# Kernel optimization log

Hardware: AMD Instinct MI355X
Metric: run time of the kernel (lower is better)

The kernel has to match this reference:

```python
import jax, jax.numpy as jnp
import numpy as np

O, T, H, W = 512, 1024, 16, 16
DIN, DP, HID, DOUT = 64, 64, 128, 128


def conv2d(x, w, b):
    # 'same' padding, stride 1, NCHW / OIHW
    ph, pw = w.shape[2] // 2, w.shape[3] // 2
    y = jax.lax.conv_general_dilated(
        x, w, (1, 1), [(ph, ph), (pw, pw)],
        dimension_numbers=('NCHW', 'OIHW', 'NCHW'))
    return y + b[None, :, None, None]


def inorm(x):
    # nn.InstanceNorm2d (affine=False), biased variance, eps=1e-5
    m = jnp.mean(x, axis=(2, 3), keepdims=True)
    v = jnp.mean((x - m) ** 2, axis=(2, 3), keepdims=True)
    return (x - m) * jax.lax.rsqrt(v + 1e-5)


def lrelu(x):
    return jnp.where(x >= 0, x, 0.1 * x)


def block(x, w, b):
    # conv -> InstanceNorm -> LeakyReLU(0.1)
    return lrelu(inorm(conv2d(x, w, b)))


def setup_inputs() -> dict:
    key = jax.random.key(0)
    ks = jax.random.split(key, 12)

    def rn(k, shape):
        fan_in = shape[1] * shape[2] * shape[3]
        return jax.random.normal(k, shape, dtype=jnp.float32) / np.sqrt(fan_in)

    return {
        'obj_maps': jax.random.normal(ks[0], (O, DIN, H, W), jnp.float32),
        'pred_vecs': jax.random.normal(ks[1], (T, DP), jnp.float32),
        'edges': jax.random.randint(ks[2], (T, 2), 0, O),
        'obj_to_img': jax.random.randint(ks[3], (O,), 0, 8),
        # net1_2d: C3 (2*DIN+DP -> HID) + IN + LReLU ; C3 (HID -> 2*HID+DOUT) no act
        'w1a': rn(ks[4], (HID, 2 * DIN + DP, 3, 3)), 'b1a': jnp.zeros((HID,), jnp.float32),
        'w1b': rn(ks[5], (2 * HID + DOUT, HID, 3, 3)), 'b1b': jnp.zeros((2 * HID + DOUT,), jnp.float32),
        # net2_2d: C3 (HID -> HID) act ; C1 (HID -> DOUT) act (non_linear_activated)
        'w2a': rn(ks[6], (HID, HID, 3, 3)), 'b2a': jnp.zeros((HID,), jnp.float32),
        'w2b': rn(ks[7], (DOUT, HID, 1, 1)), 'b2b': jnp.zeros((DOUT,), jnp.float32),
        # net_obj: C3 (DIN -> HID) act ; C1 (HID -> DOUT) act
        'woa': rn(ks[8], (HID, DIN, 3, 3)), 'boa': jnp.zeros((HID,), jnp.float32),
        'wob': rn(ks[9], (DOUT, HID, 1, 1)), 'bob': jnp.zeros((DOUT,), jnp.float32),
    }


def reference(obj_maps, pred_vecs, edges, obj_to_img,
              w1a, b1a, w1b, b1b, w2a, b2a, w2b, b2b, woa, boa, wob, bob):
    s_idx = edges[:, 0]
    o_idx = edges[:, 1]
    # pred vecs broadcast to (T, DP, H, W)
    p = jnp.broadcast_to(pred_vecs[:, :, None, None], (T, DP, H, W))
    # gather object maps by edge endpoints, concat channelwise
    t = jnp.concatenate([obj_maps[s_idx], p, obj_maps[o_idx]], axis=1)
    t = block(t, w1a, b1a)
    t = conv2d(t, w1b, b1b)  # last conv of net1_2d has no norm/activation
    new_s = t[:, :HID]                                # subject messages
    new_p = lrelu(inorm(t[:, HID:HID + DOUT]))        # self.activation branch
    new_o = t[:, HID + DOUT:]                         # object messages
    # scatter-add pooling back to objects, then average
    pooled = (jax.ops.segment_sum(new_s, s_idx, num_segments=O)
              + jax.ops.segment_sum(new_o, o_idx, num_segments=O))
    ones = jnp.ones((T,), obj_maps.dtype)
    counts = (jax.ops.segment_sum(ones, s_idx, num_segments=O)
              + jax.ops.segment_sum(ones, o_idx, num_segments=O))
    pooled = pooled / jnp.maximum(counts, 1.0)[:, None, None, None]
    new_obj = (block(block(pooled, w2a, b2a), w2b, b2b)
               + block(block(obj_maps, woa, boa), wob, bob))
    return new_obj, new_p
```

## Files before the change

kernel.cpp:

```cpp
#include <hip/hip_runtime.h>
#include <hip/hip_bf16.h>

typedef __hip_bfloat16 bf16;
typedef __attribute__((ext_vector_type(8))) short short8;
typedef __attribute__((ext_vector_type(4))) float float4v;

#define TPB 256

__device__ __forceinline__ short f2bs(float v) {
    __hip_bfloat16 h = __float2bfloat16(v);
    return *reinterpret_cast<short*>(&h);
}
__device__ __forceinline__ float bs2f(short s) {
    union { unsigned u; float f; } c; c.u = ((unsigned)(unsigned short)s) << 16; return c.f;
}
__device__ __forceinline__ short ldbits(const bf16* p, size_t i)  { return ((const short*)p)[i]; }
__device__ __forceinline__ short ldbits(const float* p, size_t i) { return f2bs(p[i]); }

__device__ __forceinline__ void gl_lds16(const void* g, void* l) {
    __builtin_amdgcn_global_load_lds(
        (const __attribute__((address_space(1))) void*)g,
        (__attribute__((address_space(3))) void*)l, 16, 0, 0);
}

__global__ void wxform_kernel(const float* __restrict__ w, bf16* __restrict__ dst,
                              int Cin, int taps, int total8) {
    int i = blockIdx.x * TPB + threadIdx.x;
    if (i >= total8) return;
    int base = i * 8;
    int nc  = Cin >> 5;
    int ci0 = base % 40;
    int r   = base / 40;
    int nn  = r & 63; r >>= 6;
    int tap = r % taps; r /= taps;
    int cb  = r % nc;
    int nb  = r / nc;
    short8 o;
#pragma unroll
    for (int j = 0; j < 8; ++j) {
        int ci = ci0 + j;
        float v = (ci < 32)
            ? w[((size_t)(nb * 64 + nn) * Cin + (cb * 32 + ci)) * taps + tap] : 0.f;
        o[j] = f2bs(v);
    }
    *(short8*)(dst + base) = o;
}

__global__ void cvt_kernel(const float* __restrict__ src, bf16* __restrict__ dst, int n8) {
    int i = blockIdx.x * TPB + threadIdx.x;
    if (i >= n8) return;
    const float4v* s = (const float4v*)src;
    float4v a = s[i * 2], b = s[i * 2 + 1];
    short8 o;
#pragma unroll
    for (int j = 0; j < 4; ++j) { o[j] = f2bs(a[j]); o[4 + j] = f2bs(b[j]); }
    *(short8*)(dst + (size_t)i * 8) = o;
}

template<int K, int MODE, bool GATHER, int NCB, typename TIN, typename TOUT>
__global__ __launch_bounds__(TPB, 2) void mconv_kernel(
    const TIN* __restrict__ in,
    const float* __restrict__ pred_vecs,
    const int*  __restrict__ edges,
    const bf16* __restrict__ wbf,
    const float* __restrict__ bfp,
    TOUT* __restrict__ out,
    bf16* __restrict__ out_s,
    bf16* __restrict__ out_o,
    int Cin, int Cout)
{
    constexpr int P    = K / 2;
    constexpr int W    = 16 + 2 * P;
    constexpr int TAPS = K * K;
    constexpr int CS   = 40;

    __shared__ __align__(16) short Ash[W * W * CS];
    __shared__ __align__(16) short Bsh[TAPS * 64 * CS];
    __shared__ float redS[256], redS2[256];

    const int tid  = threadIdx.x;
    const int lane = tid & 63;
    const int wv   = tid >> 6;
    const int quad = lane >> 4;
    const int l16  = lane & 15;

    const int d = blockIdx.x;
    const int u = (d & 7) * (gridDim.x >> 3) + (d >> 3);
    const int n  = u / NCB;
    const int n0 = (u - n * NCB) * 64;

    for (int i = tid; i < W * W * CS / 2; i += TPB) ((int*)Ash)[i] = 0;

    float4v acc[4][4];
#pragma unroll
    for (int nt = 0; nt < 4; ++nt) {
        float b = bfp[n0 + nt * 16 + l16];
#pragma unroll
        for (int mt = 0; mt < 4; ++mt) acc[mt][nt] = float4v{b, b, b, b};
    }

    int s_idx = 0, o_idx = 0;
    if (GATHER) { s_idx = edges[2 * n]; o_idx = edges[2 * n + 1]; }

    const int y0 = tid >> 4, x0 = tid & 15;
    const int abase = ((y0 + P) * W + (x0 + P)) * CS;
    const int nc = Cin >> 5;

    for (int cc0 = 0; cc0 < Cin; cc0 += 32) {
        __syncthreads();

        const char* wsrc = (const char*)wbf +
            ((size_t)(n0 >> 6) * nc + (cc0 >> 5)) * (size_t)(TAPS * 64 * CS * 2);
        for (int k = wv; k < TAPS * 5; k += 4)
            gl_lds16(wsrc + (k << 10) + (lane << 4), (char*)Bsh + (k << 10));

#pragma unroll
        for (int c8 = 0; c8 < 4; ++c8) {
            short8 pk;
#pragma unroll
            for (int j = 0; j < 8; ++j) {
                const int gc = cc0 + c8 * 8 + j;
                short s;
                if (GATHER) {
                    if (gc < 64)
                        s = ldbits(in, (size_t)s_idx * 16384 + (size_t)gc * 256 + tid);
                    else if (gc < 128)
                        s = f2bs(pred_vecs[n * 64 + (gc - 64)]);
                    else
                        s = ldbits(in, (size_t)o_idx * 16384 + (size_t)(gc - 128) * 256 + tid);
                } else {
                    s = ldbits(in, ((size_t)n * Cin + gc) * 256 + tid);
                }
                pk[j] = s;
            }
            *(short8*)&Ash[abase + c8 * 8] = pk;
        }
        __syncthreads();

#pragma unroll 1
        for (int tap = 0; tap < TAPS; ++tap) {
            const int dy = (K == 3) ? tap / 3 : 0;
            const int dx = (K == 3) ? tap - dy * 3 : 0;
            short8 bfr[4];
#pragma unroll
            for (int nt = 0; nt < 4; ++nt)
                bfr[nt] = *(const short8*)&Bsh[(tap * 64 + nt * 16 + l16) * CS + quad * 8];
#pragma unroll
            for (int mt = 0; mt < 4; ++mt) {
                const int m = (wv << 6) + mt * 16 + l16;
                const int pix = ((m >> 4) + dy) * W + ((m & 15) + dx);
                short8 afr = *(const short8*)&Ash[pix * CS + quad * 8];
#pragma unroll
                for (int nt = 0; nt < 4; ++nt)
                    acc[mt][nt] = __builtin_amdgcn_mfma_f32_16x16x32_bf16(
                        afr, bfr[nt], acc[mt][nt], 0, 0, 0);
            }
        }
    }

    const bool do_norm = (MODE == 2) ? (n0 >= 128 && n0 < 256) : true;
    float mean[4], rstd[4];
    if (do_norm) {
#pragma unroll
        for (int nt = 0; nt < 4; ++nt) {
            float s = 0.f, s2 = 0.f;
#pragma unroll
            for (int mt = 0; mt < 4; ++mt)
#pragma unroll
                for (int r = 0; r < 4; ++r) {
                    float v = acc[mt][nt][r];
                    s += v; s2 += v * v;
                }
            s  += __shfl_xor(s, 16, 64);  s  += __shfl_xor(s, 32, 64);
            s2 += __shfl_xor(s2, 16, 64); s2 += __shfl_xor(s2, 32, 64);
            if (quad == 0) {
                redS [wv * 64 + nt * 16 + l16] = s;
                redS2[wv * 64 + nt * 16 + l16] = s2;
            }
        }
        __syncthreads();
#pragma unroll
        for (int nt = 0; nt < 4; ++nt) {
            int c = nt * 16 + l16;
            float s  = redS [c] + redS [64 + c] + redS [128 + c] + redS [192 + c];
            float s2 = redS2[c] + redS2[64 + c] + redS2[128 + c] + redS2[192 + c];
            float m  = s * (1.f / 256.f);
            float var = s2 * (1.f / 256.f) - m * m;
            mean[nt] = m;
            rstd[nt] = rsqrtf(var + 1e-5f);
        }
    }

    float* Tb = (float*)Ash;
    constexpr int TS = 264;

    auto store_b = [&](bf16* base, int ch_off) {
#pragma unroll
        for (int s = 0; s < 2; ++s) {
            int task = tid + (s << 8);
            int ch = task >> 5;
            int ck = task & 31;
            const float* src = &Tb[ch * TS + (ck << 3)];
            short8 o;
#pragma unroll
            for (int j = 0; j < 8; ++j) o[j] = f2bs(src[j]);
            *(short8*)(base + (size_t)(ch_off + ch) * 256 + (ck << 3)) = o;
        }
    };
    auto store_f = [&](float* base, int ch_off, bool rmw) {
#pragma unroll
        for (int s = 0; s < 4; ++s) {
            int task = tid + (s << 8);
            int ch = task >> 6;
            int ck = task & 63;
            float4v v = *(const float4v*)&Tb[ch * TS + (ck << 2)];
            float4v* dst = (float4v*)(base + (size_t)(ch_off + ch) * 256) + ck;
            if (rmw) v = v + *dst;
            *dst = v;
        }
    };

#pragma unroll 1
    for (int nt = 0; nt < 4; ++nt) {
        __syncthreads();
#pragma unroll
        for (int mt = 0; mt < 4; ++mt)
#pragma unroll
            for (int r = 0; r < 4; ++r) {
                float v = acc[mt][nt][r];
                if (do_norm) {
                    v = (v - mean[nt]) * rstd[nt];
                    v = (v >= 0.f) ? v : 0.1f * v;
                }
                Tb[l16 * TS + (wv << 6) + mt * 16 + (quad << 2) + r] = v;
            }
        __syncthreads();
        const int nt16 = nt * 16;
        if (MODE == 2) {
            if (n0 < 128)
                store_b(out_s + (size_t)n * 128 * 256, n0 + nt16);
            else if (n0 < 256)
                store_f((float*)out + (size_t)n * 128 * 256, (n0 - 128) + nt16, false);
            else
                store_b(out_o + (size_t)n * 128 * 256, (n0 - 256) + nt16);
        } else if (MODE == 1) {
            store_f((float*)out + (size_t)n * Cout * 256, n0 + nt16, true);
        } else {
            if constexpr (sizeof(TOUT) == 2)
                store_b((bf16*)out + (size_t)n * Cout * 256, n0 + nt16);
            else
                store_f((float*)out + (size_t)n * Cout * 256, n0 + nt16, false);
        }
    }
}

__global__ __launch_bounds__(TPB) void pool_kernel(
    const int* __restrict__ edges,
    const bf16* __restrict__ new_s,
    const bf16* __restrict__ new_o,
    bf16* __restrict__ pooled)
{
    const int ob  = blockIdx.x;
    const int tid = threadIdx.x;
    __shared__ int list[2048];
    __shared__ int cnt;
    if (tid == 0) cnt = 0;
    __syncthreads();
    for (int t = tid; t < 1024; t += TPB) {
        int si = edges[2 * t], oi = edges[2 * t + 1];
        if (si == ob) { int p = atomicAdd(&cnt, 1); list[p] = t * 2; }
        if (oi == ob) { int p = atomicAdd(&cnt, 1); list[p] = t * 2 + 1; }
    }
    __syncthreads();
    const int c = cnt;
    const float inv = 1.f / fmaxf((float)c, 1.f);
    for (int e8 = tid; e8 < 4096; e8 += TPB) {
        float s[8] = {0.f, 0.f, 0.f, 0.f, 0.f, 0.f, 0.f, 0.f};
        for (int m = 0; m < c; ++m) {
            int ent = list[m];
            int nn  = ent >> 1;
            const bf16* src = (ent & 1) ? new_o : new_s;
            short8 v = *(const short8*)(src + (size_t)nn * 32768 + (size_t)e8 * 8);
#pragma unroll
            for (int j = 0; j < 8; ++j) s[j] += bs2f(v[j]);
        }
        short8 o;
#pragma unroll
        for (int j = 0; j < 8; ++j) o[j] = f2bs(s[j] * inv);
        *(short8*)(pooled + (size_t)ob * 32768 + (size_t)e8 * 8) = o;
    }
}

extern "C" void kernel_launch(void* const* d_in, const int* in_sizes, int n_in,
                              void* d_out, int out_size, void* d_ws, size_t ws_size,
                              hipStream_t stream) {
    const float* obj_maps  = (const float*)d_in[0];
    const float* pred_vecs = (const float*)d_in[1];
    const int*   edges     = (const int*)d_in[2];
    const float* w1a = (const float*)d_in[4];  const float* b1a = (const float*)d_in[5];
    const float* w1b = (const float*)d_in[6];  const float* b1b = (const float*)d_in[7];
    const float* w2a = (const float*)d_in[8];  const float* b2a = (const float*)d_in[9];
    const float* w2b = (const float*)d_in[10]; const float* b2b = (const float*)d_in[11];
    const float* woa = (const float*)d_in[12]; const float* boa = (const float*)d_in[13];
    const float* wob = (const float*)d_in[14]; const float* bob = (const float*)d_in[15];

    float* out = (float*)d_out;
    const size_t NP_OFF = (size_t)512 * 128 * 256;

    char* ws = (char*)d_ws;
    size_t off = 0;
    auto alloc = [&](size_t bytes) -> char* {
        char* p = ws + off;
        off += (bytes + 255) & ~(size_t)255;
        return p;
    };
    const size_t SZ_T = (size_t)1024 * 128 * 256 * 2;
    char* Bt1   = alloc(SZ_T);
    char* Bnews = alloc(SZ_T);
    char* Bnewo = alloc(SZ_T);
    auto wsz = [](int Cout, int Cin, int taps) -> size_t {
        return (size_t)(Cout / 64) * (Cin / 32) * taps * 64 * 40 * 2;
    };
    bf16* wb1a = (bf16*)alloc(wsz(128, 192, 9));
    bf16* wb1b = (bf16*)alloc(wsz(384, 128, 9));
    bf16* wb2a = (bf16*)alloc(wsz(128, 128, 9));
    bf16* wb2b = (bf16*)alloc(wsz(128, 128, 1));
    bf16* wboa = (bf16*)alloc(wsz(128,  64, 9));
    bf16* wbob = (bf16*)alloc(wsz(128, 128, 1));
    const size_t OBJ_SZ = (size_t)512 * 64 * 256 * 2;
    bf16* obj_bf = (bf16*)alloc(OBJ_SZ);
    const bool use_objbf = (off <= ws_size);

    bf16* t1     = (bf16*)Bt1;
    bf16* new_s  = (bf16*)Bnews;
    bf16* new_o  = (bf16*)Bnewo;
    bf16* pooled = (bf16*)Bt1;
    bf16* u1     = (bf16*)(Bt1 + (size_t)512 * 128 * 256 * 2);
    bf16* v1     = (bf16*)Bnews;

    auto wx = [&](const float* w, bf16* dw, int Cout, int Cin, int taps) {
        int total8 = (Cout / 64) * (Cin / 32) * taps * 64 * 40 / 8;
        wxform_kernel<<<dim3((total8 + TPB - 1) / TPB), dim3(TPB), 0, stream>>>(
            w, dw, Cin, taps, total8);
    };
    wx(w1a, wb1a, 128, 192, 9);
    wx(w1b, wb1b, 384, 128, 9);
    wx(w2a, wb2a, 128, 128, 9);
    wx(w2b, wb2b, 128, 128, 1);
    wx(woa, wboa, 128,  64, 9);
    wx(wob, wbob, 128, 128, 1);
    if (use_objbf)
        cvt_kernel<<<dim3(4096), dim3(TPB), 0, stream>>>(obj_maps, obj_bf, 512 * 64 * 256 / 8);

    if (use_objbf)
        mconv_kernel<3, 0, true, 2, bf16, bf16><<<dim3(2048), dim3(TPB), 0, stream>>>(
            obj_bf, pred_vecs, edges, wb1a, b1a, t1, nullptr, nullptr, 192, 128);
    else
        mconv_kernel<3, 0, true, 2, float, bf16><<<dim3(2048), dim3(TPB), 0, stream>>>(
            obj_maps, pred_vecs, edges, wb1a, b1a, t1, nullptr, nullptr, 192, 128);

    mconv_kernel<3, 2, false, 6, bf16, float><<<dim3(6144), dim3(TPB), 0, stream>>>(
        t1, nullptr, nullptr, wb1b, b1b, out + NP_OFF, new_s, new_o, 128, 384);

    pool_kernel<<<dim3(512), dim3(TPB), 0, stream>>>(edges, new_s, new_o, pooled);

    mconv_kernel<3, 0, false, 2, bf16, bf16><<<dim3(1024), dim3(TPB), 0, stream>>>(
        pooled, nullptr, nullptr, wb2a, b2a, u1, nullptr, nullptr, 128, 128);

    mconv_kernel<1, 0, false, 2, bf16, float><<<dim3(1024), dim3(TPB), 0, stream>>>(
        u1, nullptr, nullptr, wb2b, b2b, out, nullptr, nullptr, 128, 128);

    if (use_objbf)
        mconv_kernel<3, 0, false, 2, bf16, bf16><<<dim3(1024), dim3(TPB), 0, stream>>>(
            obj_bf, nullptr, nullptr, wboa, boa, v1, nullptr, nullptr, 64, 128);
    else
        mconv_kernel<3, 0, false, 2, float, bf16><<<dim3(1024), dim3(TPB), 0, stream>>>(
            obj_maps, nullptr, nullptr, wboa, boa, v1, nullptr, nullptr, 64, 128);

    mconv_kernel<1, 1, false, 2, bf16, float><<<dim3(1024), dim3(TPB), 0, stream>>>(
        v1, nullptr, nullptr, wbob, bob, out, nullptr, nullptr, 128, 128);
}
```

Measured before the change: 1.416 ms.

## Fuse scatter-add pooling into conv epilogue via float atomics

Measured after the change: 1.779 ms. 1.26x slower.

```diff
diff --git a/kernel.cpp b/kernel.cpp
--- a/kernel.cpp
+++ b/kernel.cpp
@@ -3,6 +3,7 @@
 
 typedef __hip_bfloat16 bf16;
 typedef __attribute__((ext_vector_type(8))) short short8;
+typedef __attribute__((ext_vector_type(4))) short short4v;
 typedef __attribute__((ext_vector_type(4))) float float4v;
 
 #define TPB 256
@@ -10,9 +11,6 @@
 __device__ __forceinline__ short f2bs(float v) {
     __hip_bfloat16 h = __float2bfloat16(v);
     return *reinterpret_cast<short*>(&h);
-}
-__device__ __forceinline__ float bs2f(short s) {
-    union { unsigned u; float f; } c; c.u = ((unsigned)(unsigned short)s) << 16; return c.f;
 }
 __device__ __forceinline__ short ldbits(const bf16* p, size_t i)  { return ((const short*)p)[i]; }
 __device__ __forceinline__ short ldbits(const float* p, size_t i) { return f2bs(p[i]); }
@@ -57,7 +55,21 @@
     *(short8*)(dst + (size_t)i * 8) = o;
 }
 
-template<int K, int MODE, bool GATHER, int NCB, typename TIN, typename TOUT>
+__global__ void counts_kernel(const int* __restrict__ edges, float* __restrict__ invc) {
+    __shared__ int cnt[512];
+    const int tid = threadIdx.x;
+    cnt[tid] = 0; cnt[tid + 256] = 0;
+    __syncthreads();
+    for (int t = tid; t < 1024; t += TPB) {
+        atomicAdd(&cnt[edges[2 * t]], 1);
+        atomicAdd(&cnt[edges[2 * t + 1]], 1);
+    }
+    __syncthreads();
+    invc[tid]       = 1.f / fmaxf((float)cnt[tid], 1.f);
+    invc[tid + 256] = 1.f / fmaxf((float)cnt[tid + 256], 1.f);
+}
+
+template<int K, int MODE, bool GATHER, bool SCALE, int NCB, typename TIN, typename TOUT>
 __global__ __launch_bounds__(TPB, 2) void mconv_kernel(
     const TIN* __restrict__ in,
     const float* __restrict__ pred_vecs,
@@ -65,8 +77,8 @@
     const bf16* __restrict__ wbf,
     const float* __restrict__ bfp,
     TOUT* __restrict__ out,
-    bf16* __restrict__ out_s,
-    bf16* __restrict__ out_o,
+    float* __restrict__ psum,
+    const float* __restrict__ iscale,
     int Cin, int Cout)
 {
     constexpr int P    = K / 2;
@@ -100,7 +112,9 @@
     }
 
     int s_idx = 0, o_idx = 0;
-    if (GATHER) { s_idx = edges[2 * n]; o_idx = edges[2 * n + 1]; }
+    if (GATHER || MODE == 2) { s_idx = edges[2 * n]; o_idx = edges[2 * n + 1]; }
+    float sc = 1.f;
+    if constexpr (SCALE) sc = iscale[n];
 
     const int y0 = tid >> 4, x0 = tid & 15;
     const int abase = ((y0 + P) * W + (x0 + P)) * CS;
@@ -128,6 +142,8 @@
                         s = f2bs(pred_vecs[n * 64 + (gc - 64)]);
                     else
                         s = ldbits(in, (size_t)o_idx * 16384 + (size_t)(gc - 128) * 256 + tid);
+                } else if (SCALE) {
+                    s = f2bs(((const float*)in)[((size_t)n * Cin + gc) * 256 + tid] * sc);
                 } else {
                     s = ldbits(in, ((size_t)n * Cin + gc) * 256 + tid);
                 }
@@ -192,31 +208,37 @@
     }
 
     float* Tb = (float*)Ash;
-    constexpr int TS = 264;
+    constexpr int TS = 260;
 
     auto store_b = [&](bf16* base, int ch_off) {
 #pragma unroll
-        for (int s = 0; s < 2; ++s) {
-            int task = tid + (s << 8);
-            int ch = task >> 5;
-            int ck = task & 31;
-            const float* src = &Tb[ch * TS + (ck << 3)];
-            short8 o;
-#pragma unroll
-            for (int j = 0; j < 8; ++j) o[j] = f2bs(src[j]);
-            *(short8*)(base + (size_t)(ch_off + ch) * 256 + (ck << 3)) = o;
+        for (int s = 0; s < 4; ++s) {
+            const int ch = (s << 2) + wv;
+            const float* src = &Tb[ch * TS + (lane << 2)];
+            short4v o4;
+#pragma unroll
+            for (int j = 0; j < 4; ++j) o4[j] = f2bs(src[j]);
+            *(short4v*)(base + (size_t)(ch_off + ch) * 256 + (lane << 2)) = o4;
         }
     };
     auto store_f = [&](float* base, int ch_off, bool rmw) {
 #pragma unroll
         for (int s = 0; s < 4; ++s) {
-            int task = tid + (s << 8);
-            int ch = task >> 6;
-            int ck = task & 63;
-            float4v v = *(const float4v*)&Tb[ch * TS + (ck << 2)];
-            float4v* dst = (float4v*)(base + (size_t)(ch_off + ch) * 256) + ck;
+            const int ch = (s << 2) + wv;
+            float4v v = *(const float4v*)&Tb[ch * TS + (lane << 2)];
+            float4v* dst = (float4v*)(base + (size_t)(ch_off + ch) * 256) + lane;
             if (rmw) v = v + *dst;
             *dst = v;
+        }
+    };
+    auto atomic_f = [&](float* base, int ch_off) {
+#pragma unroll
+        for (int s = 0; s < 4; ++s) {
+            const int ch = (s << 2) + wv;
+            const float* src = &Tb[ch * TS + (lane << 2)];
+            float* dst = base + (size_t)(ch_off + ch) * 256 + (lane << 2);
+#pragma unroll
+            for (int j = 0; j < 4; ++j) atomicAdd(dst + j, src[j]);
         }
     };
 
@@ -238,11 +260,11 @@
         const int nt16 = nt * 16;
         if (MODE == 2) {
             if (n0 < 128)
-                store_b(out_s + (size_t)n * 128 * 256, n0 + nt16);
+                atomic_f(psum + (size_t)s_idx * 128 * 256, n0 + nt16);
             else if (n0 < 256)
                 store_f((float*)out + (size_t)n * 128 * 256, (n0 - 128) + nt16, false);
             else
-                store_b(out_o + (size_t)n * 128 * 256, (n0 - 256) + nt16);
+                atomic_f(psum + (size_t)o_idx * 128 * 256, (n0 - 256) + nt16);
         } else if (MODE == 1) {
             store_f((float*)out + (size_t)n * Cout * 256, n0 + nt16, true);
         } else {
@@ -251,43 +273,6 @@
             else
                 store_f((float*)out + (size_t)n * Cout * 256, n0 + nt16, false);
         }
-    }
-}
-
-__global__ __launch_bounds__(TPB) void pool_kernel(
-    const int* __restrict__ edges,
-    const bf16* __restrict__ new_s,
-    const bf16* __restrict__ new_o,
-    bf16* __restrict__ pooled)
-{
-    const int ob  = blockIdx.x;
-    const int tid = threadIdx.x;
-    __shared__ int list[2048];
-    __shared__ int cnt;
-    if (tid == 0) cnt = 0;
-    __syncthreads();
-    for (int t = tid; t < 1024; t += TPB) {
-        int si = edges[2 * t], oi = edges[2 * t + 1];
-        if (si == ob) { int p = atomicAdd(&cnt, 1); list[p] = t * 2; }
-        if (oi == ob) { int p = atomicAdd(&cnt, 1); list[p] = t * 2 + 1; }
-    }
-    __syncthreads();
-    const int c = cnt;
-    const float inv = 1.f / fmaxf((float)c, 1.f);
-    for (int e8 = tid; e8 < 4096; e8 += TPB) {
-        float s[8] = {0.f, 0.f, 0.f, 0.f, 0.f, 0.f, 0.f, 0.f};
-        for (int m = 0; m < c; ++m) {
-            int ent = list[m];
-            int nn  = ent >> 1;
-            const bf16* src = (ent & 1) ? new_o : new_s;
-            short8 v = *(const short8*)(src + (size_t)nn * 32768 + (size_t)e8 * 8);
-#pragma unroll
-            for (int j = 0; j < 8; ++j) s[j] += bs2f(v[j]);
-        }
-        short8 o;
-#pragma unroll
-        for (int j = 0; j < 8; ++j) o[j] = f2bs(s[j] * inv);
-        *(short8*)(pooled + (size_t)ob * 32768 + (size_t)e8 * 8) = o;
     }
 }
 
@@ -316,8 +301,8 @@
     };
     const size_t SZ_T = (size_t)1024 * 128 * 256 * 2;
     char* Bt1   = alloc(SZ_T);
-    char* Bnews = alloc(SZ_T);
-    char* Bnewo = alloc(SZ_T);
+    char* Bpsum = alloc((size_t)512 * 128 * 256 * 4);
+    char* Bu1   = alloc((size_t)512 * 128 * 256 * 2);
     auto wsz = [](int Cout, int Cin, int taps) -> size_t {
         return (size_t)(Cout / 64) * (Cin / 32) * taps * 64 * 40 * 2;
     };
@@ -327,17 +312,17 @@
     bf16* wb2b = (bf16*)alloc(wsz(128, 128, 1));
     bf16* wboa = (bf16*)alloc(wsz(128,  64, 9));
     bf16* wbob = (bf16*)alloc(wsz(128, 128, 1));
+    float* invc = (float*)alloc(512 * 4);
     const size_t OBJ_SZ = (size_t)512 * 64 * 256 * 2;
     bf16* obj_bf = (bf16*)alloc(OBJ_SZ);
     const bool use_objbf = (off <= ws_size);
 
-    bf16* t1     = (bf16*)Bt1;
-    bf16* new_s  = (bf16*)Bnews;
-    bf16* new_o  = (bf16*)Bnewo;
-    bf16* pooled = (bf16*)Bt1;
-    bf16* u1     = (bf16*)(Bt1 + (size_t)512 * 128 * 256 * 2);
-    bf16* v1     = (bf16*)Bnews;
-
+    bf16*  t1   = (bf16*)Bt1;
+    float* psum = (float*)Bpsum;
+    bf16*  u1   = (bf16*)Bu1;
+    bf16*  v1   = (bf16*)Bt1;
+
+    hipMemsetAsync(psum, 0, (size_t)512 * 128 * 256 * 4, stream);
     auto wx = [&](const float* w, bf16* dw, int Cout, int Cin, int taps) {
         int total8 = (Cout / 64) * (Cin / 32) * taps * 64 * 40 / 8;
         wxform_kernel<<<dim3((total8 + TPB - 1) / TPB), dim3(TPB), 0, stream>>>(
@@ -349,34 +334,33 @@
     wx(w2b, wb2b, 128, 128, 1);
     wx(woa, wboa, 128,  64, 9);
     wx(wob, wbob, 128, 128, 1);
+    counts_kernel<<<dim3(1), dim3(TPB), 0, stream>>>(edges, invc);
     if (use_objbf)
         cvt_kernel<<<dim3(4096), dim3(TPB), 0, stream>>>(obj_maps, obj_bf, 512 * 64 * 256 / 8);
 
     if (use_objbf)
-        mconv_kernel<3, 0, true, 2, bf16, bf16><<<dim3(2048), dim3(TPB), 0, stream>>>(
+        mconv_kernel<3, 0, true, false, 2, bf16, bf16><<<dim3(2048), dim3(TPB), 0, stream>>>(
             obj_bf, pred_vecs, edges, wb1a, b1a, t1, nullptr, nullptr, 192, 128);
     else
-        mconv_kernel<3, 0, true, 2, float, bf16><<<dim3(2048), dim3(TPB), 0, stream>>>(
+        mconv_kernel<3, 0, true, false, 2, float, bf16><<<dim3(2048), dim3(TPB), 0, stream>>>(
             obj_maps, pred_vecs, edges, wb1a, b1a, t1, nullptr, nullptr, 192, 128);
 
-    mconv_kernel<3, 2, false, 6, bf16, float><<<dim3(6144), dim3(TPB), 0, stream>>>(
-        t1, nullptr, nullptr, wb1b, b1b, out + NP_OFF, new_s, new_o, 128, 384);
-
-    pool_kernel<<<dim3(512), dim3(TPB), 0, stream>>>(edges, new_s, new_o, pooled);
-
-    mconv_kernel<3, 0, false, 2, bf16, bf16><<<dim3(1024), dim3(TPB), 0, stream>>>(
-        pooled, nullptr, nullptr, wb2a, b2a, u1, nullptr, nullptr, 128, 128);
-
-    mconv_kernel<1, 0, false, 2, bf16, float><<<dim3(1024), dim3(TPB), 0, stream>>>(
+    mconv_kernel<3, 2, false, false, 6, bf16, float><<<dim3(6144), dim3(TPB), 0, stream>>>(
+        t1, nullptr, edges, wb1b, b1b, out + NP_OFF, psum, nullptr, 128, 384);
+
+    mconv_kernel<3, 0, false, true, 2, float, bf16><<<dim3(1024), dim3(TPB), 0, stream>>>(
+        psum, nullptr, nullptr, wb2a, b2a, u1, nullptr, invc, 128, 128);
+
+    mconv_kernel<1, 0, false, false, 2, bf16, float><<<dim3(1024), dim3(TPB), 0, stream>>>(
         u1, nullptr, nullptr, wb2b, b2b, out, nullptr, nullptr, 128, 128);
 
     if (use_objbf)
-        mconv_kernel<3, 0, false, 2, bf16, bf16><<<dim3(1024), dim3(TPB), 0, stream>>>(
+        mconv_kernel<3, 0, false, false, 2, bf16, bf16><<<dim3(1024), dim3(TPB), 0, stream>>>(
             obj_bf, nullptr, nullptr, wboa, boa, v1, nullptr, nullptr, 64, 128);
     else
-        mconv_kernel<3, 0, false, 2, float, bf16><<<dim3(1024), dim3(TPB), 0, stream>>>(
+        mconv_kernel<3, 0, false, false, 2, float, bf16><<<dim3(1024), dim3(TPB), 0, stream>>>(
             obj_maps, nullptr, nullptr, wboa, boa, v1, nullptr, nullptr, 64, 128);
 
-    mconv_kernel<1, 1, false, 2, bf16, float><<<dim3(1024), dim3(TPB), 0, stream>>>(
+    mconv_kernel<1, 1, false, false, 2, bf16, float><<<dim3(1024), dim3(TPB), 0, stream>>>(
         v1, nullptr, nullptr, wbob, bob, out, nullptr, nullptr, 128, 128);
 }
```

## Stream conv weights per tap-row with double-buffered LDS and raise occupancy

Applied to the files above, without the earlier changes.

Measured after the change: 2.203 ms. 1.56x slower.

```diff
diff --git a/kernel.cpp b/kernel.cpp
--- a/kernel.cpp
+++ b/kernel.cpp
@@ -3,6 +3,7 @@
 
 typedef __hip_bfloat16 bf16;
 typedef __attribute__((ext_vector_type(8))) short short8;
+typedef __attribute__((ext_vector_type(4))) short short4v;
 typedef __attribute__((ext_vector_type(4))) float float4v;
 
 #define TPB 256
@@ -16,6 +17,8 @@
 }
 __device__ __forceinline__ short ldbits(const bf16* p, size_t i)  { return ((const short*)p)[i]; }
 __device__ __forceinline__ short ldbits(const float* p, size_t i) { return f2bs(p[i]); }
+__device__ __forceinline__ void stf(float* p, size_t i, float v) { p[i] = v; }
+__device__ __forceinline__ void stf(bf16* p, size_t i, float v)  { p[i] = __float2bfloat16(v); }
 
 __device__ __forceinline__ void gl_lds16(const void* g, void* l) {
     __builtin_amdgcn_global_load_lds(
@@ -24,26 +27,36 @@
 }
 
 __global__ void wxform_kernel(const float* __restrict__ w, bf16* __restrict__ dst,
-                              int Cin, int taps, int total8) {
+                              int Cin, int K, int total8) {
     int i = blockIdx.x * TPB + threadIdx.x;
     if (i >= total8) return;
-    int base = i * 8;
-    int nc  = Cin >> 5;
-    int ci0 = base % 40;
-    int r   = base / 40;
-    int nn  = r & 63; r >>= 6;
-    int tap = r % taps; r /= taps;
-    int cb  = r % nc;
-    int nb  = r / nc;
+    const int NGR  = (K == 3) ? 3 : 1;
+    const int GRPB = (K == 3) ? 14336 : 5120;
+    const int RAWB = (K == 3) ? 13824 : 4608;
+    const int TAPS = K * K;
+    const int nc   = Cin >> 5;
+    long b   = (long)i * 16;
+    int  gl  = (int)(b / GRPB);
+    int  off = (int)(b - (long)gl * GRPB);
+    int  g   = gl % NGR; int t2 = gl / NGR;
+    int  cb  = t2 % nc;  int nb = t2 / nc;
     short8 o;
 #pragma unroll
     for (int j = 0; j < 8; ++j) {
-        int ci = ci0 + j;
-        float v = (ci < 32)
-            ? w[((size_t)(nb * 64 + nn) * Cin + (cb * 32 + ci)) * taps + tap] : 0.f;
+        int ob = off + j * 2;
+        float v = 0.f;
+        if (ob < RAWB) {
+            int r  = ob / 72;
+            int ci = (ob - r * 72) >> 1;
+            if (ci < 32) {
+                int tap = g * ((K == 3) ? 3 : 1) + (r >> 6);
+                int nn  = r & 63;
+                v = w[((size_t)(nb * 64 + nn) * Cin + (cb * 32 + ci)) * TAPS + tap];
+            }
+        }
         o[j] = f2bs(v);
     }
-    *(short8*)(dst + base) = o;
+    *(short8*)((char*)dst + b) = o;
 }
 
 __global__ void cvt_kernel(const float* __restrict__ src, bf16* __restrict__ dst, int n8) {
@@ -58,7 +71,7 @@
 }
 
 template<int K, int MODE, bool GATHER, int NCB, typename TIN, typename TOUT>
-__global__ __launch_bounds__(TPB, 2) void mconv_kernel(
+__global__ __launch_bounds__(TPB, 3) void mconv_kernel(
     const TIN* __restrict__ in,
     const float* __restrict__ pred_vecs,
     const int*  __restrict__ edges,
@@ -71,11 +84,14 @@
 {
     constexpr int P    = K / 2;
     constexpr int W    = 16 + 2 * P;
-    constexpr int TAPS = K * K;
-    constexpr int CS   = 40;
+    constexpr int NGR  = (K == 3) ? 3 : 1;
+    constexpr int TPG  = (K == 3) ? 3 : 1;
+    constexpr int GRPB = (K == 3) ? 14336 : 5120;
+    constexpr int NBUF = (K == 3) ? 2 : 1;
+    constexpr int CS   = 36;
 
     __shared__ __align__(16) short Ash[W * W * CS];
-    __shared__ __align__(16) short Bsh[TAPS * 64 * CS];
+    __shared__ __align__(16) short Bsh[NBUF][GRPB / 2];
     __shared__ float redS[256], redS2[256];
 
     const int tid  = threadIdx.x;
@@ -106,20 +122,15 @@
     const int abase = ((y0 + P) * W + (x0 + P)) * CS;
     const int nc = Cin >> 5;
 
-    for (int cc0 = 0; cc0 < Cin; cc0 += 32) {
+    for (int cc = 0; cc < nc; ++cc) {
         __syncthreads();
-
-        const char* wsrc = (const char*)wbf +
-            ((size_t)(n0 >> 6) * nc + (cc0 >> 5)) * (size_t)(TAPS * 64 * CS * 2);
-        for (int k = wv; k < TAPS * 5; k += 4)
-            gl_lds16(wsrc + (k << 10) + (lane << 4), (char*)Bsh + (k << 10));
 
 #pragma unroll
         for (int c8 = 0; c8 < 4; ++c8) {
             short8 pk;
 #pragma unroll
             for (int j = 0; j < 8; ++j) {
-                const int gc = cc0 + c8 * 8 + j;
+                const int gc = cc * 32 + c8 * 8 + j;
                 short s;
                 if (GATHER) {
                     if (gc < 64)
@@ -135,26 +146,40 @@
             }
             *(short8*)&Ash[abase + c8 * 8] = pk;
         }
+
+        const char* bimg = (const char*)wbf +
+            (size_t)((n0 >> 6) * nc + cc) * (NGR * GRPB);
+        for (int k = wv; k < GRPB / 1024; k += 4)
+            gl_lds16(bimg + (k << 10) + (lane << 4), (char*)Bsh[0] + (k << 10));
         __syncthreads();
 
 #pragma unroll 1
-        for (int tap = 0; tap < TAPS; ++tap) {
-            const int dy = (K == 3) ? tap / 3 : 0;
-            const int dx = (K == 3) ? tap - dy * 3 : 0;
-            short8 bfr[4];
-#pragma unroll
-            for (int nt = 0; nt < 4; ++nt)
-                bfr[nt] = *(const short8*)&Bsh[(tap * 64 + nt * 16 + l16) * CS + quad * 8];
-#pragma unroll
-            for (int mt = 0; mt < 4; ++mt) {
-                const int m = (wv << 6) + mt * 16 + l16;
-                const int pix = ((m >> 4) + dy) * W + ((m & 15) + dx);
-                short8 afr = *(const short8*)&Ash[pix * CS + quad * 8];
+        for (int g = 0; g < NGR; ++g) {
+            if (NGR > 1 && g + 1 < NGR) {
+                const char* bs2 = bimg + (size_t)(g + 1) * GRPB;
+                for (int k = wv; k < GRPB / 1024; k += 4)
+                    gl_lds16(bs2 + (k << 10) + (lane << 4),
+                             (char*)Bsh[(g + 1) & (NBUF - 1)] + (k << 10));
+            }
+            const short* Bb = Bsh[(NBUF > 1) ? (g & 1) : 0];
+#pragma unroll
+            for (int t = 0; t < TPG; ++t) {
+                short8 bfr[4];
 #pragma unroll
                 for (int nt = 0; nt < 4; ++nt)
-                    acc[mt][nt] = __builtin_amdgcn_mfma_f32_16x16x32_bf16(
-                        afr, bfr[nt], acc[mt][nt], 0, 0, 0);
-            }
+                    bfr[nt] = *(const short8*)&Bb[(t * 64 + nt * 16 + l16) * CS + quad * 8];
+#pragma unroll
+                for (int mt = 0; mt < 4; ++mt) {
+                    const int m = (wv << 6) + mt * 16 + l16;
+                    const int pix = ((m >> 4) + g) * W + ((m & 15) + t);
+                    short8 afr = *(const short8*)&Ash[pix * CS + quad * 8];
+#pragma unroll
+                    for (int nt = 0; nt < 4; ++nt)
+                        acc[mt][nt] = __builtin_amdgcn_mfma_f32_16x16x32_bf16(
+                            afr, bfr[nt], acc[mt][nt], 0, 0, 0);
+                }
+            }
+            if (NGR > 1 && g + 1 < NGR) __syncthreads();
         }
     }
 
@@ -192,29 +217,25 @@
     }
 
     float* Tb = (float*)Ash;
-    constexpr int TS = 264;
+    constexpr int TS = 260;
 
     auto store_b = [&](bf16* base, int ch_off) {
 #pragma unroll
-        for (int s = 0; s < 2; ++s) {
-            int task = tid + (s << 8);
-            int ch = task >> 5;
-            int ck = task & 31;
-            const float* src = &Tb[ch * TS + (ck << 3)];
-            short8 o;
-#pragma unroll
-            for (int j = 0; j < 8; ++j) o[j] = f2bs(src[j]);
-            *(short8*)(base + (size_t)(ch_off + ch) * 256 + (ck << 3)) = o;
+        for (int s = 0; s < 4; ++s) {
+            const int ch = (s << 2) + wv;
+            const float* src = &Tb[ch * TS + (lane << 2)];
+            short4v o4;
+#pragma unroll
+            for (int j = 0; j < 4; ++j) o4[j] = f2bs(src[j]);
+            *(short4v*)(base + (size_t)(ch_off + ch) * 256 + (lane << 2)) = o4;
         }
     };
     auto store_f = [&](float* base, int ch_off, bool rmw) {
 #pragma unroll
         for (int s = 0; s < 4; ++s) {
-            int task = tid + (s << 8);
-            int ch = task >> 6;
-            int ck = task & 63;
-            float4v v = *(const float4v*)&Tb[ch * TS + (ck << 2)];
-            float4v* dst = (float4v*)(base + (size_t)(ch_off + ch) * 256) + ck;
+            const int ch = (s << 2) + wv;
+            float4v v = *(const float4v*)&Tb[ch * TS + (lane << 2)];
+            float4v* dst = (float4v*)(base + (size_t)(ch_off + ch) * 256) + lane;
             if (rmw) v = v + *dst;
             *dst = v;
         }
@@ -318,14 +339,14 @@
     char* Bt1   = alloc(SZ_T);
     char* Bnews = alloc(SZ_T);
     char* Bnewo = alloc(SZ_T);
-    auto wsz = [](int Cout, int Cin, int taps) -> size_t {
-        return (size_t)(Cout / 64) * (Cin / 32) * taps * 64 * 40 * 2;
+    auto wsz = [](int Cout, int Cin, int K) -> size_t {
+        return (size_t)(Cout / 64) * (Cin / 32) * ((K == 3) ? 3 * 14336 : 5120);
     };
-    bf16* wb1a = (bf16*)alloc(wsz(128, 192, 9));
-    bf16* wb1b = (bf16*)alloc(wsz(384, 128, 9));
-    bf16* wb2a = (bf16*)alloc(wsz(128, 128, 9));
+    bf16* wb1a = (bf16*)alloc(wsz(128, 192, 3));
+    bf16* wb1b = (bf16*)alloc(wsz(384, 128, 3));
+    bf16* wb2a = (bf16*)alloc(wsz(128, 128, 3));
     bf16* wb2b = (bf16*)alloc(wsz(128, 128, 1));
-    bf16* wboa = (bf16*)alloc(wsz(128,  64, 9));
+    bf16* wboa = (bf16*)alloc(wsz(128,  64, 3));
     bf16* wbob = (bf16*)alloc(wsz(128, 128, 1));
     const size_t OBJ_SZ = (size_t)512 * 64 * 256 * 2;
     bf16* obj_bf = (bf16*)alloc(OBJ_SZ);
@@ -338,16 +359,16 @@
     bf16* u1     = (bf16*)(Bt1 + (size_t)512 * 128 * 256 * 2);
     bf16* v1     = (bf16*)Bnews;
 
-    auto wx = [&](const float* w, bf16* dw, int Cout, int Cin, int taps) {
-        int total8 = (Cout / 64) * (Cin / 32) * taps * 64 * 40 / 8;
+    auto wx = [&](const float* w, bf16* dw, int Cout, int Cin, int K) {
+        int total8 = (int)(wsz(Cout, Cin, K) / 16);
         wxform_kernel<<<dim3((total8 + TPB - 1) / TPB), dim3(TPB), 0, stream>>>(
-            w, dw, Cin, taps, total8);
+            w, dw, Cin, K, total8);
     };
-    wx(w1a, wb1a, 128, 192, 9);
-    wx(w1b, wb1b, 384, 128, 9);
-    wx(w2a, wb2a, 128, 128, 9);
+    wx(w1a, wb1a, 128, 192, 3);
+    wx(w1b, wb1b, 384, 128, 3);
+    wx(w2a, wb2a, 128, 128, 3);
     wx(w2b, wb2b, 128, 128, 1);
-    wx(woa, wboa, 128,  64, 9);
+    wx(woa, wboa, 128,  64, 3);
     wx(wob, wbob, 128, 128, 1);
     if (use_objbf)
         cvt_kernel<<<dim3(4096), dim3(TPB), 0, stream>>>(obj_maps, obj_bf, 512 * 64 * 256 / 8);
```
